# Kernel tuning notes

Measured on AMD Instinct MI355X. Metric: run time of the kernel, lower is better.

## Reference

```python
import jax, jax.numpy as jnp
import numpy as np

FEATURES = 256
CODES = 8192


def setup_inputs() -> dict:
    key = jax.random.key(0)
    kz, kc = jax.random.split(key)
    z = jax.random.normal(kz, (16, FEATURES, 32, 32), dtype=jnp.float32)
    # codebook initialized as randn(codes, features) / features in the original
    codebook = jax.random.normal(kc, (CODES, FEATURES), dtype=jnp.float32) / FEATURES
    return {"z": z, "codebook": codebook}


def reference(z, codebook):
    # z: [B, C, H, W]; codebook: [K, C]
    B, C, H, W = z.shape
    # 'b c h w -> (b h w) c'
    zf = jnp.transpose(z, (0, 2, 3, 1)).reshape(-1, C)  # [N, C], N = B*H*W
    # squared euclidean distances via expansion: |z|^2 - 2 z.cb^T + |cb|^2
    dist = zf @ (-2.0 * codebook.T)                      # [N, K]
    dist = dist + jnp.sum(zf * zf, axis=1, keepdims=True)
    dist = dist + jnp.sum(codebook * codebook, axis=1)[None, :]
    idx = jnp.argmin(dist, axis=1)                       # [N]
    idx = idx.reshape(B, H, W)                           # [B, H, W]
    # encode: codebook gather, then 'b h w c -> b c h w'
    zq = jnp.transpose(codebook[idx], (0, 3, 1, 2))      # [B, C, H, W]
    # eval mode: no stochastic mixing (training-only branch omitted)
    return zq, idx
```

## Files before the change

### kernel.cpp

```cpp
#include <hip/hip_runtime.h>
#include <stdint.h>

#define FEAT 256
#define CODES 8192
#define NQ 16384
#define ZQ_ELEMS (NQ * FEAT)
#define MARGIN 2e-3f
#define RM_ERR 1.0e-3f
#define NSLICE 8
#define CAP_PAIRS (1 << 18)
#define KSC (-0.0078125f)
#define MEMO_OFF 31457280ull
#define MEMO_BYTES 67108864ull

typedef _Float16 f16x8 __attribute__((ext_vector_type(8)));
typedef float f32x4 __attribute__((ext_vector_type(4)));

__device__ __forceinline__ void async_lds16(void* lds, const void* g) {
  __builtin_amdgcn_global_load_lds(
      (const __attribute__((address_space(1))) void*)(uintptr_t)(g),
      (__attribute__((address_space(3))) void*)(uint32_t)(uintptr_t)(lds),
      16, 0, 0);
}

__device__ __forceinline__ unsigned f2mono(float v) {
  unsigned u = __float_as_uint(v);
  return (u & 0x80000000u) ? ~u : (u | 0x80000000u);
}
__device__ __forceinline__ float mono2f(unsigned t) {
  unsigned u = (t & 0x80000000u) ? (t & 0x7fffffffu) : ~t;
  return __uint_as_float(u);
}
__device__ __forceinline__ unsigned pack_f16x2(float a, float b) {
  unsigned short ha = __builtin_bit_cast(unsigned short, (_Float16)a);
  unsigned short hb = __builtin_bit_cast(unsigned short, (_Float16)b);
  return (unsigned)ha | ((unsigned)hb << 16);
}

template <int STRIDE>
__device__ __forceinline__ float pairwise256_sq(const float* __restrict__ base, int lane16) {
  const int h = lane16 >> 3, j = lane16 & 7;
  const float* p = base + (h * 128 + j) * STRIDE;
  float x = p[0];
  float r = __fmul_rn(x, x);
#pragma unroll
  for (int i = 1; i < 16; ++i) {
    float y = p[i * 8 * STRIDE];
    r = __fadd_rn(r, __fmul_rn(y, y));
  }
  r = __fadd_rn(r, __shfl_xor(r, 1, 64));
  r = __fadd_rn(r, __shfl_xor(r, 2, 64));
  r = __fadd_rn(r, __shfl_xor(r, 4, 64));
  float other = __shfl_xor(r, 8, 64);
  float lo = (h == 0) ? r : other;
  float hi = (h == 0) ? other : r;
  return __fadd_rn(lo, hi);
}

#define PREP_BLOCKS 2112
__global__ __launch_bounds__(256) void prep(const float* __restrict__ cb,
                                            const float* __restrict__ z,
                                            float* __restrict__ cbnorm,
                                            char* __restrict__ At, float* __restrict__ zT,
                                            char* __restrict__ Bt,
                                            unsigned* __restrict__ gmin,
                                            unsigned long long* __restrict__ packed,
                                            int* __restrict__ paircount) {
  __shared__ __align__(16) char smem[128 * 40 * 2 + 128 * 36 * 4];
  const int bb0 = blockIdx.x;
  const int t = threadIdx.x;
  if (bb0 < 512) {
    const int g = (bb0 * 256 + t) >> 4;
    const int lane16 = t & 15;
    float v = pairwise256_sq<1>(cb + g * FEAT, lane16);
    if (lane16 == 0) cbnorm[g] = v;
  } else if (bb0 < 1536) {
    _Float16* T = (_Float16*)smem;
    float* Tf = (float*)(smem + 128 * 40 * 2);
    const int blk = bb0 - 512;
    const int mt = blk >> 3, ct = blk & 7;
    const int q0 = mt * 128, bb = q0 >> 10, hw0 = q0 & 1023;
    const int c0 = ct * 32;
#pragma unroll
    for (int it = 0; it < 16; ++it) {
      const int cc = it * 2 + (t >> 7);
      const int qi = t & 127;
      float v = z[bb * (FEAT * 1024) + (c0 + cc) * 1024 + hw0 + qi];
      T[qi * 40 + cc] = (_Float16)v;
      Tf[qi * 36 + cc] = v;
    }
    __syncthreads();
    const int r = t >> 1, h = t & 1;
    {
      float4 a = *(const float4*)&T[r * 40 + h * 16];
      float4 b = *(const float4*)&T[r * 40 + h * 16 + 8];
      char* dst = At + (size_t)(mt * 8 + ct) * 8192 + t * 32;
      *(float4*)dst = a;
      *(float4*)(dst + 16) = b;
    }
    float* zrow = zT + (size_t)(q0 + r) * FEAT + c0 + h * 16;
#pragma unroll
    for (int e = 0; e < 4; ++e)
      *(float4*)(zrow + e * 4) = *(const float4*)&Tf[r * 36 + h * 16 + e * 4];
  } else if (bb0 < 2048) {
    const int T4 = (bb0 - 1536) * 256 + t;
    const int K = T4 >> 4, part = T4 & 15;
    const float* src = cb + (size_t)K * FEAT + part * 16;
    const int nt = K >> 7, rem = K & 127;
    const int wn = rem >> 6, j = (rem >> 4) & 3, llo = rem & 15;
#pragma unroll
    for (int g = 0; g < 2; ++g) {
      const int c0 = part * 16 + g * 8;
      const int ct = c0 >> 5, lhi = (c0 >> 3) & 3;
      const int cg = nt * 8 + ct;
      f16x8 o;
#pragma unroll
      for (int e = 0; e < 8; ++e) o[e] = (_Float16)(src[g * 8 + e] * 256.0f);
      const size_t s = ((size_t)((cg * 2 + wn) * 4 + j) << 6) + (size_t)(lhi * 16 + llo);
      *(f16x8*)(Bt + s * 16) = o;
    }
  } else {
    const int bi = bb0 - 2048;
    const int idx = bi * 256 + t;
    gmin[idx] = 0xFFFFFFFFu;
    packed[idx] = ~0ull;
    if (bi == 0 && t < 64) paircount[t] = 0;
  }
}

__global__ __launch_bounds__(256) void znorm_zt(const float* __restrict__ zT,
                                                float* __restrict__ znorm) {
  const int q = (blockIdx.x * 256 + threadIdx.x) >> 4;
  const int lane16 = threadIdx.x & 15;
  float v = pairwise256_sq<1>(zT + (size_t)q * FEAT, lane16);
  if (lane16 == 0) znorm[q] = v;
}

template <int PASS>
__device__ __forceinline__ void gemm_body(const char* __restrict__ At,
                                          const char* __restrict__ Bt,
                                          const float* __restrict__ cbnorm,
                                          unsigned* __restrict__ gmin,
                                          unsigned* __restrict__ pairs,
                                          int* __restrict__ paircount,
                                          unsigned* __restrict__ memo) {
  __shared__ __align__(16) char Af[65536];
  __shared__ __align__(16) char Bs0[8192];
  __shared__ __align__(16) char Bs1[8192];

  const int tid = threadIdx.x;
  const int slice = blockIdx.x & 7, mt = blockIdx.x >> 3;
  const int wave = tid >> 6, lane = tid & 63;
  const int wm = wave >> 1, wn = wave & 1;
  const int col = lane & 15, quad = lane >> 4;

  const int srow = wave * 32 + (lane >> 2);
  const int ss = lane & 3;
  const char* Abase = At + (size_t)(mt * 8) * 8192;
  const char* Bslice = Bt + (size_t)slice * 524288;

#pragma unroll
  for (int ct = 0; ct < 8; ++ct) {
#pragma unroll
    for (int i = 0; i < 2; ++i) {
      const int r = srow + i * 16;
      const int cs = ss ^ ((r >> 1) & 3);
      async_lds16(Af + ct * 8192 + wave * 2048 + i * 1024,
                  Abase + (size_t)ct * 8192 + r * 64 + cs * 16);
    }
  }

#define STAGE_B(BUF, CIDX)                                                          \
  do {                                                                              \
    const char* gs_ = Bslice + ((size_t)(CIDX) << 13) + wave * 2048 + lane * 16;    \
    async_lds16((BUF) + wave * 2048, gs_);                                          \
    async_lds16((BUF) + wave * 2048 + 1024, gs_ + 1024);                            \
  } while (0)

  STAGE_B(Bs0, 0);
  STAGE_B(Bs1, 1);

  int aoff[4];
#pragma unroll
  for (int i = 0; i < 4; ++i) {
    const int m = wm * 64 + i * 16 + col;
    aoff[i] = m * 64 + ((quad ^ ((m >> 1) & 3)) << 4);
  }

  int qrow[16];
#pragma unroll
  for (int row = 0; row < 16; ++row)
    qrow[row] = mt * 128 + wm * 64 + (row >> 2) * 16 + quad * 4 + (row & 3);

  float vmin[16], thr[16];
#pragma unroll
  for (int row = 0; row < 16; ++row) vmin[row] = 3.4e38f;
  if (PASS == 1) {
#pragma unroll
    for (int row = 0; row < 16; ++row) thr[row] = mono2f(gmin[qrow[row]]) + MARGIN;
  }

  f32x4 acc[4][4];

  __syncthreads();

#define CHUNK(CT, STG, CNEXT, WMODE)                                                \
  do {                                                                              \
    char* Bcur_ = ((CT) & 1) ? Bs1 : Bs0;                                           \
    f16x8 bf_[4], af_[4];                                                           \
    _Pragma("unroll") for (int j = 0; j < 4; ++j)                                   \
        bf_[j] = *(const f16x8*)(Bcur_ + wn * 4096 + j * 1024 + lane * 16);         \
    _Pragma("unroll") for (int i = 0; i < 4; ++i)                                   \
        af_[i] = *(const f16x8*)(Af + (CT) * 8192 + aoff[i]);                       \
    asm volatile("s_waitcnt lgkmcnt(0)" ::: "memory");                              \
    __builtin_amdgcn_sched_barrier(0);                                              \
    __builtin_amdgcn_s_barrier();                 \
    if (STG) {                                                                      \
      STAGE_B(Bcur_, CNEXT);                                                        \
      __builtin_amdgcn_sched_barrier(0);         \
    }                                                                               \
    _Pragma("unroll") for (int i = 0; i < 4; ++i)                                   \
        _Pragma("unroll") for (int j = 0; j < 4; ++j)                               \
            acc[i][j] = __builtin_amdgcn_mfma_f32_16x16x32_f16(af_[i], bf_[j],      \
                                                               acc[i][j], 0, 0, 0); \
    if ((WMODE) == 2) {                                                             \
      asm volatile("s_waitcnt vmcnt(2)" ::: "memory");                              \
      __builtin_amdgcn_sched_barrier(0);                                            \
    }                                                                               \
    if ((WMODE) == 0) {                                                             \
      asm volatile("s_waitcnt vmcnt(0)" ::: "memory");                              \
      __builtin_amdgcn_sched_barrier(0);                                            \
    }                                                                               \
    __builtin_amdgcn_s_barrier();             \
  } while (0)

#define ZEROACC                                                                     \
  do {                                                                              \
    _Pragma("unroll") for (int i = 0; i < 4; ++i)                                   \
        _Pragma("unroll") for (int j = 0; j < 4; ++j)                               \
            acc[i][j] = (f32x4){0.f, 0.f, 0.f, 0.f};                                \
  } while (0)

#define SCORING(NT)                                                                 \
  do {                                                                              \
    const int k0_ = (slice * 8 + (NT)) * 128;                                       \
    float cn_[4];                                                                   \
    _Pragma("unroll") for (int j = 0; j < 4; ++j)                                   \
        cn_[j] = cbnorm[k0_ + wn * 64 + j * 16 + col];                              \
    unsigned* sb_ = (PASS == 3)                                                     \
        ? memo + ((((unsigned)blockIdx.x * 8u + (unsigned)(NT)) * 4u +              \
                   (unsigned)wave) * 8u) * 64u + (unsigned)lane                     \
        : nullptr;                                                                  \
    float prev_ = 0.f;                                                              \
    _Pragma("unroll") for (int i = 0; i < 4; ++i)                                   \
        _Pragma("unroll") for (int r = 0; r < 4; ++r) {                             \
      const int row_ = i * 4 + r;                                                   \
      const float s0_ = __builtin_fmaf(acc[i][0][r], KSC, cn_[0]);                  \
      const float s1_ = __builtin_fmaf(acc[i][1][r], KSC, cn_[1]);                  \
      const float s2_ = __builtin_fmaf(acc[i][2][r], KSC, cn_[2]);                  \
      const float s3_ = __builtin_fmaf(acc[i][3][r], KSC, cn_[3]);                  \
      const float rm_ = fminf(fminf(s0_, s1_), fminf(s2_, s3_));                    \
      if (PASS != 1) {                                                              \
        vmin[row_] = fminf(vmin[row_], rm_);                                        \
        if (PASS == 3) {                                                            \
          if ((r & 1) == 0) prev_ = rm_;                                            \
          else sb_[(unsigned)((i * 2 + (r >> 1)) * 64)] = pack_f16x2(prev_, rm_);   \
        }                                                                           \
      } else if (rm_ <= thr[row_]) {      \
        const float sv_[4] = {s0_, s1_, s2_, s3_};                                  \
        _Pragma("unroll") for (int j = 0; j < 4; ++j) {                             \
          if (sv_[j] <= thr[row_]) {                                                \
            const int slot_ = atomicAdd(paircount, 1);                              \
            if (slot_ < CAP_PAIRS)                                                  \
              pairs[slot_] = ((unsigned)qrow[row_] << 13) |                         \
                             (unsigned)(k0_ + wn * 64 + j * 16 + col);              \
          }                                                                         \
        }                                                                           \
      }                                                                             \
    }                                                                               \
  } while (0)

  for (int nt = 0; nt < 7; ++nt) {
    ZEROACC;
#pragma unroll
    for (int ct = 0; ct < 8; ++ct) CHUNK(ct, true, nt * 8 + ct + 2, 2);
    SCORING(nt);
  }
  ZEROACC;
  CHUNK(0, true, 58, 2);
  CHUNK(1, true, 59, 2);
  CHUNK(2, true, 60, 2);
  CHUNK(3, true, 61, 2);
  CHUNK(4, true, 62, 2);
  CHUNK(5, true, 63, 2);
  CHUNK(6, false, 0, 0);
  CHUNK(7, false, 0, 3);
  SCORING(7);

#undef STAGE_B
#undef CHUNK
#undef ZEROACC
#undef SCORING

  if (PASS != 1) {
#pragma unroll
    for (int row = 0; row < 16; ++row) {
      float v = vmin[row];
      v = fminf(v, __shfl_xor(v, 1, 64));
      v = fminf(v, __shfl_xor(v, 2, 64));
      v = fminf(v, __shfl_xor(v, 4, 64));
      v = fminf(v, __shfl_xor(v, 8, 64));
      if (col == 0) atomicMin(&gmin[qrow[row]], f2mono(v));
    }
  }
}

__global__ __launch_bounds__(256, 2) void gemm_pass1(const char* __restrict__ At,
                                                     const char* __restrict__ Bt,
                                                     const float* __restrict__ cbnorm,
                                                     unsigned* __restrict__ gmin) {
  gemm_body<0>(At, Bt, cbnorm, gmin, nullptr, nullptr, nullptr);
}

__global__ __launch_bounds__(256, 2) void gemm_pass1m(const char* __restrict__ At,
                                                      const char* __restrict__ Bt,
                                                      const float* __restrict__ cbnorm,
                                                      unsigned* __restrict__ gmin,
                                                      unsigned* __restrict__ memo) {
  gemm_body<3>(At, Bt, cbnorm, gmin, nullptr, nullptr, memo);
}

__global__ __launch_bounds__(256, 2) void gemm_pass2(const char* __restrict__ At,
                                                     const char* __restrict__ Bt,
                                                     const float* __restrict__ cbnorm,
                                                     unsigned* __restrict__ gmin,
                                                     unsigned* __restrict__ pairs,
                                                     int* __restrict__ paircount) {
  gemm_body<1>(At, Bt, cbnorm, gmin, pairs, paircount, nullptr);
}

__global__ __launch_bounds__(256) void scan_exact(const unsigned* __restrict__ memo,
                                                  const unsigned* __restrict__ gmin,
                                                  const float* __restrict__ zT,
                                                  const float* __restrict__ cb,
                                                  const float* __restrict__ cbnorm,
                                                  const float* __restrict__ znorm,
                                                  unsigned long long* __restrict__ packed) {
  const unsigned NU4 = 4194304u;
  const unsigned stride = gridDim.x * blockDim.x;
  const int lane = threadIdx.x & 63;
  for (unsigned U = blockIdx.x * 256 + threadIdx.x; U < NU4; U += stride) {
    const uint4 v = ((const uint4*)memo)[U];
    const unsigned u = U << 2;
    const unsigned lane0 = u & 63, col0 = lane0 & 15, quad = lane0 >> 4;
    const unsigned rp = (u >> 6) & 7;
    const unsigned w = (u >> 9) & 3;
    const unsigned t = (u >> 11) & 7;
    const unsigned blk = u >> 14;
    const unsigned mt = blk >> 3, slice = blk & 7;
    const unsigned wm = w >> 1, wn = w & 1;
    const unsigned ntile = slice * 8u + t;
    const unsigned row0 = rp * 2u;
    const int q0 = (int)(mt * 128u + wm * 64u + (row0 >> 2) * 16u + quad * 4u + (row0 & 3u));
    const float thr0 = mono2f(gmin[q0]) + (MARGIN + RM_ERR);
    const float thr1 = mono2f(gmin[q0 + 1]) + (MARGIN + RM_ERR);
    const unsigned wv[4] = {v.x, v.y, v.z, v.w};
    unsigned hm = 0;
#pragma unroll
    for (int wi = 0; wi < 4; ++wi) {
      const float lo = (float)__builtin_bit_cast(_Float16, (unsigned short)(wv[wi] & 0xffffu));
      const float hi = (float)__builtin_bit_cast(_Float16, (unsigned short)(wv[wi] >> 16));
      if (lo <= thr0) hm |= 1u << (wi * 2);
      if (hi <= thr1) hm |= 1u << (wi * 2 + 1);
    }
    while (true) {
      const unsigned long long act = __ballot(hm != 0);
      if (!act) break;
      const int src = (int)(__ffsll((unsigned long long)act) - 1);
      unsigned myid = 0;
      {
        const int bit = __ffs((int)hm) - 1;
        if (bit >= 0) {
          const unsigned wi = (unsigned)bit >> 1, h = (unsigned)bit & 1;
          const unsigned kid = (ntile << 5) | (wn << 4) | (col0 + wi);
          myid = ((unsigned)(q0 + (int)h) << 11) | kid;
        }
      }
      const unsigned id = (unsigned)__shfl((int)myid, src, 64);
      const int q = (int)(id >> 11);
      const int base = (int)(((id >> 5) & 63u) * 128u + ((id >> 4) & 1u) * 64u + (id & 15u));
      const float4 zv = ((const float4*)(zT + (size_t)q * FEAT))[lane];
      const float zn = znorm[q];
      unsigned long long best = ~0ull;
#pragma unroll
      for (int j = 0; j < 4; ++j) {
        const int k = base + j * 16;
        const float4 cv = ((const float4*)(cb + (size_t)k * FEAT))[lane];
        float d = __builtin_fmaf(zv.w, cv.w,
                  __builtin_fmaf(zv.z, cv.z,
                  __builtin_fmaf(zv.y, cv.y, __fmul_rn(zv.x, cv.x))));
#pragma unroll
        for (int dd = 1; dd < 64; dd <<= 1) d = __fadd_rn(d, __shfl_xor(d, dd, 64));
        const float s = __fadd_rn(__fadd_rn(__fmul_rn(-2.0f, d), zn), cbnorm[k]);
        const unsigned long long key = ((unsigned long long)f2mono(s) << 32) | (unsigned)k;
        best = (key < best) ? key : best;
      }
      if (lane == 0) atomicMin(&packed[q], best);
      if (lane == src) hm &= hm - 1;
    }
  }
}

__global__ __launch_bounds__(256) void exact_cand(const float* __restrict__ zT,
                                                  const float* __restrict__ cb,
                                                  const float* __restrict__ cbnorm,
                                                  const float* __restrict__ znorm,
                                                  const unsigned* __restrict__ pairs,
                                                  const int* __restrict__ paircount,
                                                  unsigned long long* __restrict__ packed) {
  const int cnt = min(*paircount, CAP_PAIRS);
  const int gw = (blockIdx.x * 256 + threadIdx.x) >> 6;
  const int nw = (gridDim.x * 256) >> 6;
  const int lane = threadIdx.x & 63;
  for (int p = gw; p < cnt; p += nw) {
    const unsigned qk = pairs[p];
    const int q = qk >> 13, k = qk & 8191;
    const float4 cv = ((const float4*)(cb + (size_t)k * FEAT))[lane];
    const float4 zv = ((const float4*)(zT + (size_t)q * FEAT))[lane];
    float d = __builtin_fmaf(zv.w, cv.w,
              __builtin_fmaf(zv.z, cv.z,
              __builtin_fmaf(zv.y, cv.y, __fmul_rn(zv.x, cv.x))));
#pragma unroll
    for (int dd = 1; dd < 64; dd <<= 1) d = __fadd_rn(d, __shfl_xor(d, dd, 64));
    const float s = __fadd_rn(__fadd_rn(__fmul_rn(-2.0f, d), znorm[q]), cbnorm[k]);
    if (lane == 0) {
      const unsigned long long key = ((unsigned long long)f2mono(s) << 32) | (unsigned)k;
      atomicMin(&packed[q], key);
    }
  }
}

__global__ __launch_bounds__(256) void vq_gather(const float* __restrict__ cb,
                                                 const unsigned long long* __restrict__ packed,
                                                 float* __restrict__ out) {
  const int q0 = blockIdx.x * 64;
  const int nl = threadIdx.x & 63;
  const int cg = threadIdx.x >> 6;
  const int q = q0 + nl;
  const int kq = (int)((unsigned)packed[q] & 8191u);
  const int b = q >> 10, hw = q & 1023;
  const float4* cb4 = (const float4*)cb;
#pragma unroll
  for (int t = 0; t < 16; ++t) {
    const int cc = cg + t * 4;
    const float4 v = cb4[kq * 64 + cc];
    const int base = b * (FEAT * 1024) + (cc * 4) * 1024 + hw;
    out[base] = v.x;
    out[base + 1024] = v.y;
    out[base + 2048] = v.z;
    out[base + 3072] = v.w;
  }
  if (threadIdx.x < 64) {
    const int qq = q0 + threadIdx.x;
    out[ZQ_ELEMS + qq] = (float)(int)((unsigned)packed[qq] & 8191u);
  }
}

extern "C" void kernel_launch(void* const* d_in, const int* in_sizes, int n_in,
                              void* d_out, int out_size, void* d_ws, size_t ws_size,
                              hipStream_t stream) {
  const float* z = (const float*)d_in[0];
  const float* cb = (const float*)d_in[1];
  char* w = (char*)d_ws;
  char* At = w;
  char* Bt = w + 8388608;
  float* zT = (float*)(w + 12582912);
  float* cbnorm = (float*)(w + 29360128);
  float* znorm = (float*)(w + 29392896);
  unsigned* gmin = (unsigned*)(w + 29458432);
  int* paircount = (int*)(w + 29523968);
  unsigned* pairs = (unsigned*)(w + 29524224);
  unsigned long long* packed = (unsigned long long*)(w + 30572800);
  unsigned* memo = (unsigned*)(w + MEMO_OFF);

  const bool use_memo = ws_size >= (size_t)(MEMO_OFF + MEMO_BYTES);

  prep<<<PREP_BLOCKS, 256, 0, stream>>>(cb, z, cbnorm, At, zT, Bt,
                                        gmin, packed, paircount);
  znorm_zt<<<NQ / 16, 256, 0, stream>>>(zT, znorm);
  if (use_memo) {
    gemm_pass1m<<<(NQ / 128) * NSLICE, 256, 0, stream>>>(At, Bt, cbnorm, gmin, memo);
    scan_exact<<<2048, 256, 0, stream>>>(memo, gmin, zT, cb, cbnorm, znorm, packed);
  } else {
    gemm_pass1<<<(NQ / 128) * NSLICE, 256, 0, stream>>>(At, Bt, cbnorm, gmin);
    gemm_pass2<<<(NQ / 128) * NSLICE, 256, 0, stream>>>(At, Bt, cbnorm, gmin, pairs, paircount);
    exact_cand<<<512, 256, 0, stream>>>(zT, cb, cbnorm, znorm, pairs, paircount, packed);
  }
  vq_gather<<<NQ / 64, 256, 0, stream>>>(cb, packed, (float*)d_out);
}
```

Before: 187.4 us.

## Hold A fragments in registers and use four-slot B ring with one barrier

The prep kernel now writes A tiles in MFMA fragment order, so each lane loads its A operands straight from global memory into registers once, and the 64KB A staging area in LDS goes away. B staging moves from a double buffer to a four-slot ring with a prefetch depth of three. The stage is issued before the wait, which removes one barrier per chunk. This frees a lot of LDS and cuts LDS reads and barriers, at the cost of many more VGPRs (32 f16x8 fragments per lane), which may reduce occupancy.

```diff
diff --git a/kernel.cpp b/kernel.cpp
--- a/kernel.cpp
+++ b/kernel.cpp
@@ -90,14 +90,16 @@
       Tf[qi * 36 + cc] = v;
     }
     __syncthreads();
+#pragma unroll
+    for (int g2 = 0; g2 < 2; ++g2) {
+      const int f = t * 2 + g2;
+      const int fwm = f >> 8, fi = (f >> 6) & 3, fl = f & 63;
+      const int row = fwm * 64 + fi * 16 + (fl & 15);
+      const int kg = fl >> 4;
+      const float4 frag = *(const float4*)&T[row * 40 + kg * 8];
+      *(float4*)(At + (size_t)(mt * 8 + ct) * 8192 + (size_t)f * 16) = frag;
+    }
     const int r = t >> 1, h = t & 1;
-    {
-      float4 a = *(const float4*)&T[r * 40 + h * 16];
-      float4 b = *(const float4*)&T[r * 40 + h * 16 + 8];
-      char* dst = At + (size_t)(mt * 8 + ct) * 8192 + t * 32;
-      *(float4*)dst = a;
-      *(float4*)(dst + 16) = b;
-    }
     float* zrow = zT + (size_t)(q0 + r) * FEAT + c0 + h * 16;
 #pragma unroll
     for (int e = 0; e < 4; ++e)
@@ -144,9 +146,7 @@
                                           unsigned* __restrict__ pairs,
                                           int* __restrict__ paircount,
                                           unsigned* __restrict__ memo) {
-  __shared__ __align__(16) char Af[65536];
-  __shared__ __align__(16) char Bs0[8192];
-  __shared__ __align__(16) char Bs1[8192];
+  __shared__ __align__(16) char Bs[4][8192];
 
   const int tid = threadIdx.x;
   const int slice = blockIdx.x & 7, mt = blockIdx.x >> 3;
@@ -154,75 +154,65 @@
   const int wm = wave >> 1, wn = wave & 1;
   const int col = lane & 15, quad = lane >> 4;
 
-  const int srow = wave * 32 + (lane >> 2);
-  const int ss = lane & 3;
   const char* Abase = At + (size_t)(mt * 8) * 8192;
   const char* Bslice = Bt + (size_t)slice * 524288;
 
-#pragma unroll
-  for (int ct = 0; ct < 8; ++ct) {
-#pragma unroll
-    for (int i = 0; i < 2; ++i) {
-      const int r = srow + i * 16;
-      const int cs = ss ^ ((r >> 1) & 3);
-      async_lds16(Af + ct * 8192 + wave * 2048 + i * 1024,
-                  Abase + (size_t)ct * 8192 + r * 64 + cs * 16);
-    }
-  }
-
-#define STAGE_B(BUF, CIDX)                                                          \
+  int qrow[16];
+#pragma unroll
+  for (int row = 0; row < 16; ++row)
+    qrow[row] = mt * 128 + wm * 64 + (row >> 2) * 16 + quad * 4 + (row & 3);
+
+  float vmin[16], thr[16];
+#pragma unroll
+  for (int row = 0; row < 16; ++row) vmin[row] = 3.4e38f;
+  if (PASS == 1) {
+#pragma unroll
+    for (int row = 0; row < 16; ++row) thr[row] = mono2f(gmin[qrow[row]]) + MARGIN;
+  }
+
+  f16x8 af[8][4];
+#pragma unroll
+  for (int ct = 0; ct < 8; ++ct)
+#pragma unroll
+    for (int i = 0; i < 4; ++i)
+      af[ct][i] = *(const f16x8*)(Abase + (size_t)ct * 8192 +
+                                  (size_t)(wm * 256 + i * 64 + lane) * 16);
+
+#define STAGE_B(SLOT, CIDX)                                                         \
   do {                                                                              \
     const char* gs_ = Bslice + ((size_t)(CIDX) << 13) + wave * 2048 + lane * 16;    \
-    async_lds16((BUF) + wave * 2048, gs_);                                          \
-    async_lds16((BUF) + wave * 2048 + 1024, gs_ + 1024);                            \
+    async_lds16(Bs[SLOT] + wave * 2048, gs_);                                       \
+    async_lds16(Bs[SLOT] + wave * 2048 + 1024, gs_ + 1024);                         \
   } while (0)
 
-  STAGE_B(Bs0, 0);
-  STAGE_B(Bs1, 1);
-
-  int aoff[4];
-#pragma unroll
-  for (int i = 0; i < 4; ++i) {
-    const int m = wm * 64 + i * 16 + col;
-    aoff[i] = m * 64 + ((quad ^ ((m >> 1) & 3)) << 4);
-  }
-
-  int qrow[16];
-#pragma unroll
-  for (int row = 0; row < 16; ++row)
-    qrow[row] = mt * 128 + wm * 64 + (row >> 2) * 16 + quad * 4 + (row & 3);
-
-  float vmin[16], thr[16];
-#pragma unroll
-  for (int row = 0; row < 16; ++row) vmin[row] = 3.4e38f;
-  if (PASS == 1) {
-#pragma unroll
-    for (int row = 0; row < 16; ++row) thr[row] = mono2f(gmin[qrow[row]]) + MARGIN;
-  }
+  STAGE_B(0, 0);
+  STAGE_B(1, 1);
+  STAGE_B(2, 2);
+  asm volatile("s_waitcnt vmcnt(4)" ::: "memory");
+  __builtin_amdgcn_sched_barrier(0);
+  __builtin_amdgcn_s_barrier();
 
   f32x4 acc[4][4];
-
-  __syncthreads();
 
 #define CHUNK(CT, STG, CNEXT, WMODE)                                                \
   do {                                                                              \
-    char* Bcur_ = ((CT) & 1) ? Bs1 : Bs0;                                           \
-    f16x8 bf_[4], af_[4];                                                           \
+    f16x8 bf_[4];                                                                   \
     _Pragma("unroll") for (int j = 0; j < 4; ++j)                                   \
-        bf_[j] = *(const f16x8*)(Bcur_ + wn * 4096 + j * 1024 + lane * 16);         \
-    _Pragma("unroll") for (int i = 0; i < 4; ++i)                                   \
-        af_[i] = *(const f16x8*)(Af + (CT) * 8192 + aoff[i]);                       \
+        bf_[j] = *(const f16x8*)(Bs[(CT) & 3] + wn * 4096 + j * 1024 + lane * 16);  \
+    if (STG) {                                                                      \
+      STAGE_B((CNEXT) & 3, CNEXT);                                                  \
+      __builtin_amdgcn_sched_barrier(0);                                            \
+    }                                                                               \
     asm volatile("s_waitcnt lgkmcnt(0)" ::: "memory");                              \
     __builtin_amdgcn_sched_barrier(0);                                              \
-    __builtin_amdgcn_s_barrier();                 \
-    if (STG) {                                                                      \
-      STAGE_B(Bcur_, CNEXT);                                                        \
-      __builtin_amdgcn_sched_barrier(0);         \
-    }                                                                               \
     _Pragma("unroll") for (int i = 0; i < 4; ++i)                                   \
         _Pragma("unroll") for (int j = 0; j < 4; ++j)                               \
-            acc[i][j] = __builtin_amdgcn_mfma_f32_16x16x32_f16(af_[i], bf_[j],      \
+            acc[i][j] = __builtin_amdgcn_mfma_f32_16x16x32_f16(af[CT][i], bf_[j],   \
                                                                acc[i][j], 0, 0, 0); \
+    if ((WMODE) == 4) {                                                             \
+      asm volatile("s_waitcnt vmcnt(4)" ::: "memory");                              \
+      __builtin_amdgcn_sched_barrier(0);                                            \
+    }                                                                               \
     if ((WMODE) == 2) {                                                             \
       asm volatile("s_waitcnt vmcnt(2)" ::: "memory");                              \
       __builtin_amdgcn_sched_barrier(0);                                            \
@@ -231,7 +221,7 @@
       asm volatile("s_waitcnt vmcnt(0)" ::: "memory");                              \
       __builtin_amdgcn_sched_barrier(0);                                            \
     }                                                                               \
-    __builtin_amdgcn_s_barrier();             \
+    __builtin_amdgcn_s_barrier();                                                   \
   } while (0)
 
 #define ZEROACC                                                                     \
@@ -283,16 +273,16 @@
   for (int nt = 0; nt < 7; ++nt) {
     ZEROACC;
 #pragma unroll
-    for (int ct = 0; ct < 8; ++ct) CHUNK(ct, true, nt * 8 + ct + 2, 2);
+    for (int ct = 0; ct < 8; ++ct) CHUNK(ct, true, nt * 8 + ct + 3, 4);
     SCORING(nt);
   }
   ZEROACC;
-  CHUNK(0, true, 58, 2);
-  CHUNK(1, true, 59, 2);
-  CHUNK(2, true, 60, 2);
-  CHUNK(3, true, 61, 2);
-  CHUNK(4, true, 62, 2);
-  CHUNK(5, true, 63, 2);
+  CHUNK(0, true, 59, 4);
+  CHUNK(1, true, 60, 4);
+  CHUNK(2, true, 61, 4);
+  CHUNK(3, true, 62, 4);
+  CHUNK(4, true, 63, 4);
+  CHUNK(5, false, 0, 2);
   CHUNK(6, false, 0, 0);
   CHUNK(7, false, 0, 3);
   SCORING(7);
```

After: 182.2 us. 1.03x faster.
